# Performance work log

Measured on AMD Instinct MI355X. Metric: run time of the kernel, lower is better.

## Reference

```python
import jax, jax.numpy as jnp
import numpy as np
from jax.scipy.special import gammaln

N_VOXELS = 500_000
SPATIAL_DIM = 256
N_STUDY = 1000
MOD_DIM = 64


def setup_inputs() -> dict:
    key = jax.random.key(0)
    ks = jax.random.split(key, 8)
    coef_spline_bases = jax.random.uniform(ks[0], (N_VOXELS, SPATIAL_DIM), dtype=jnp.float32)
    moderators_g0 = jax.random.uniform(ks[1], (N_STUDY, MOD_DIM), dtype=jnp.float32)
    moderators_g1 = jax.random.uniform(ks[2], (N_STUDY, MOD_DIM), dtype=jnp.float32)
    foci_per_voxel_g0 = jax.random.randint(ks[3], (N_VOXELS, 1), 0, 4).astype(jnp.float32)
    foci_per_voxel_g1 = jax.random.randint(ks[4], (N_VOXELS, 1), 0, 4).astype(jnp.float32)
    # Linear weights init: uniform(-0.01, 0.01) as in the torch module
    spatial_coef = jax.random.uniform(ks[5], (2, SPATIAL_DIM), dtype=jnp.float32, minval=-0.01, maxval=0.01)
    moderators_coef = jax.random.uniform(ks[6], (1, MOD_DIM), dtype=jnp.float32, minval=-0.01, maxval=0.01)
    # overdispersion init 0.01 -> sqrt = 0.1 per group
    overdispersion_sqrt = jnp.full((2,), 0.1, dtype=jnp.float32)
    return {
        "coef_spline_bases": coef_spline_bases,
        "moderators_g0": moderators_g0,
        "moderators_g1": moderators_g1,
        "foci_per_voxel_g0": foci_per_voxel_g0,
        "foci_per_voxel_g1": foci_per_voxel_g1,
        "spatial_coef": spatial_coef,
        "moderators_coef": moderators_coef,
        "overdispersion_sqrt": overdispersion_sqrt,
    }


def _three_term(y, r):
    # Fused, vectorized equivalent of the per-count python loop:
    # every voxel with y >= 1 contributes lgamma(y+r) - lgamma(y+1) - lgamma(r) exactly once.
    terms = gammaln(y + r) - gammaln(y + 1.0) - gammaln(jnp.broadcast_to(r, y.shape))
    return jnp.sum(jnp.where(y > 0, terms, 0.0))


def _group_log_l(coef_spline_bases, w_spatial, moderators, wm, y, s):
    # w_spatial: [D], wm: [1, M], y: [V, 1], s: scalar overdispersion_sqrt
    v = 1.0 / (s * s)                                    # 1 / overdispersion
    mu_spatial = jnp.exp(coef_spline_bases @ w_spatial[:, None])   # [V, 1]
    mu_mod = jnp.exp(moderators @ wm.T)                  # [S, 1]
    sum_m = jnp.sum(mu_mod)
    sum_m2 = jnp.sum(mu_mod ** 2)
    numerator = mu_spatial ** 2 * sum_m2                 # [V, 1]
    denominator = mu_spatial ** 2 * sum_m ** 2           # [V, 1]
    p = numerator / (v * mu_spatial * sum_m + numerator) # [V, 1]
    r = v * denominator / numerator                      # [V, 1] (constant per group)
    return _three_term(y, r) + jnp.sum(r * jnp.log(1.0 - p) + y * jnp.log(p))


def reference(coef_spline_bases, moderators_g0, moderators_g1,
              foci_per_voxel_g0, foci_per_voxel_g1,
              spatial_coef, moderators_coef, overdispersion_sqrt):
    ll0 = _group_log_l(coef_spline_bases, spatial_coef[0], moderators_g0,
                       moderators_coef, foci_per_voxel_g0, overdispersion_sqrt[0])
    ll1 = _group_log_l(coef_spline_bases, spatial_coef[1], moderators_g1,
                       moderators_coef, foci_per_voxel_g1, overdispersion_sqrt[1])
    return -(ll0 + ll1)
```

## Files before the change

### kernel.cpp

```cpp
#include <hip/hip_runtime.h>
#include <math.h>

#define NV 500000
#define SD 256
#define NS 1000
#define MD 64

__global__ void prep_kernel(const float* __restrict__ mod0,
                            const float* __restrict__ mod1,
                            const float* __restrict__ wm,
                            const float* __restrict__ over,
                            double* __restrict__ acc,
                            float* __restrict__ sc) {
    __shared__ float s_wm[MD];
    __shared__ float4 buf[256];
    const int tid = threadIdx.x;
    if (tid < MD) s_wm[tid] = wm[tid];
    __syncthreads();

    float sm0 = 0.f, sq0 = 0.f, sm1 = 0.f, sq1 = 0.f;
    for (int j = tid; j < NS; j += 256) {
        const float* r0 = mod0 + j * MD;
        const float* r1 = mod1 + j * MD;
        float d0 = 0.f, d1 = 0.f;
        #pragma unroll 8
        for (int k = 0; k < MD; ++k) {
            d0 += r0[k] * s_wm[k];
            d1 += r1[k] * s_wm[k];
        }
        float m0 = expf(d0), m1 = expf(d1);
        sm0 += m0; sq0 += m0 * m0;
        sm1 += m1; sq1 += m1 * m1;
    }
    buf[tid] = make_float4(sm0, sq0, sm1, sq1);
    __syncthreads();
    for (int s = 128; s > 0; s >>= 1) {
        if (tid < s) {
            float4 a = buf[tid], b = buf[tid + s];
            buf[tid] = make_float4(a.x + b.x, a.y + b.y, a.z + b.z, a.w + b.w);
        }
        __syncthreads();
    }
    if (tid == 0) {
        const float4 t = buf[0];
        const float summ[2] = { t.x, t.z };
        const float sumq[2] = { t.y, t.w };
        for (int g = 0; g < 2; ++g) {
            const float s_ = over[g];
            const float v  = 1.0f / (s_ * s_);
            const float r  = v * summ[g] * summ[g] / sumq[g];
            sc[g * 8 + 0] = v;
            sc[g * 8 + 1] = summ[g];
            sc[g * 8 + 2] = sumq[g];
            sc[g * 8 + 3] = r;
            const float lgr = lgammaf(r);
            sc[g * 8 + 4] = 0.0f;
            sc[g * 8 + 5] = lgammaf(1.0f + r) - lgammaf(2.0f) - lgr;
            sc[g * 8 + 6] = lgammaf(2.0f + r) - lgammaf(3.0f) - lgr;
            sc[g * 8 + 7] = lgammaf(3.0f + r) - lgammaf(4.0f) - lgr;
        }
        acc[0] = 0.0;
    }
}

__global__ void main_kernel(const float* __restrict__ csb,
                            const float* __restrict__ f0,
                            const float* __restrict__ f1,
                            const float* __restrict__ spatial,
                            const float* __restrict__ sc,
                            double* __restrict__ acc) {
    const int lane = threadIdx.x & 63;
    const int wib  = threadIdx.x >> 6;
    const int gw   = blockIdx.x * (blockDim.x >> 6) + wib;
    const int nw   = gridDim.x * (blockDim.x >> 6);

    const float4 w0 = reinterpret_cast<const float4*>(spatial)[lane];
    const float4 w1 = reinterpret_cast<const float4*>(spatial + SD)[lane];

    const float v0 = sc[0],  smA = sc[1],  sqA = sc[2],  rA = sc[3];
    const float tA1 = sc[5], tA2 = sc[6],  tA3 = sc[7];
    const float v1 = sc[8],  smB = sc[9],  sqB = sc[10], rB = sc[11];
    const float tB1 = sc[13], tB2 = sc[14], tB3 = sc[15];

    double accl = 0.0;
    const int nchunks = (NV + 63) >> 6;
    for (int c = gw; c < nchunks; c += nw) {
        const int base = c << 6;
        const float* rowbase = csb + (size_t)base * SD;
        float dot0 = 0.0f, dot1 = 0.0f;
        #pragma unroll 4
        for (int j = 0; j < 64; ++j) {
            float d0 = 0.0f, d1 = 0.0f;
            if (base + j < NV) {
                const float4 a = *(reinterpret_cast<const float4*>(rowbase + (size_t)j * SD) + lane);
                d0 = a.x * w0.x + a.y * w0.y + a.z * w0.z + a.w * w0.w;
                d1 = a.x * w1.x + a.y * w1.y + a.z * w1.z + a.w * w1.w;
            }
            #pragma unroll
            for (int off = 32; off > 0; off >>= 1) {
                d0 += __shfl_xor(d0, off, 64);
                d1 += __shfl_xor(d1, off, 64);
            }
            if (lane == j) { dot0 = d0; dot1 = d1; }
        }
        const int vox = base + lane;
        if (vox < NV) {
            const float y0 = f0[vox];
            const float y1 = f1[vox];
            float mu  = expf(dot0);
            float num = mu * mu * sqA;
            float den = v0 * mu * smA + num;
            float p   = num / den;
            int   yi  = (int)y0;
            float tt  = (yi == 1) ? tA1 : (yi == 2) ? tA2 : (yi == 3) ? tA3 : 0.0f;
            const float c0 = rA * logf(1.0f - p) + y0 * logf(p) + tt;
            mu  = expf(dot1);
            num = mu * mu * sqB;
            den = v1 * mu * smB + num;
            p   = num / den;
            yi  = (int)y1;
            tt  = (yi == 1) ? tB1 : (yi == 2) ? tB2 : (yi == 3) ? tB3 : 0.0f;
            const float c1 = rB * logf(1.0f - p) + y1 * logf(p) + tt;
            accl += (double)c0 + (double)c1;
        }
    }

    __shared__ double sred[256];
    sred[threadIdx.x] = accl;
    __syncthreads();
    for (int s = 128; s > 0; s >>= 1) {
        if (threadIdx.x < s) sred[threadIdx.x] += sred[threadIdx.x + s];
        __syncthreads();
    }
    if (threadIdx.x == 0) {
        unsafeAtomicAdd(acc, sred[0]);
    }
}

__global__ void fin_kernel(const double* __restrict__ acc, float* __restrict__ out) {
    if (threadIdx.x == 0 && blockIdx.x == 0) out[0] = -(float)acc[0];
}

extern "C" void kernel_launch(void* const* d_in, const int* in_sizes, int n_in,
                              void* d_out, int out_size, void* d_ws, size_t ws_size,
                              hipStream_t stream) {
    const float* csb     = (const float*)d_in[0];
    const float* mod0    = (const float*)d_in[1];
    const float* mod1    = (const float*)d_in[2];
    const float* f0      = (const float*)d_in[3];
    const float* f1      = (const float*)d_in[4];
    const float* spatial = (const float*)d_in[5];
    const float* wm      = (const float*)d_in[6];
    const float* over    = (const float*)d_in[7];
    float*  out = (float*)d_out;
    double* acc = (double*)d_ws;
    float*  sc  = (float*)((char*)d_ws + 16);

    prep_kernel<<<1, 256, 0, stream>>>(mod0, mod1, wm, over, acc, sc);
    main_kernel<<<2048, 256, 0, stream>>>(csb, f0, f1, spatial, sc, acc);
    fin_kernel<<<1, 64, 0, stream>>>(acc, out);
}
```

Baseline: 704.0 us.

## Split each row across 4 lanes to cut cross-lane shuffle reductions

Changes the dot-product mapping so each group of 4 lanes handles one voxel row (16 rows per pass, 4 passes per 64-row chunk), with weights staged in LDS. This replaces 64 full 6-step wave reductions per chunk with 2-step partial reductions plus a gather shuffle, cutting shuffle/ALU overhead in a memory-bound loop. In exchange, each lane's loads now stride within a row rather than being fully coalesced across the wave, and weights are read from LDS every iteration.

Result: no change. 708.9 us (+0.7%).

```diff
diff --git a/kernel.cpp b/kernel.cpp
--- a/kernel.cpp
+++ b/kernel.cpp
@@ -69,13 +69,24 @@
                             const float* __restrict__ spatial,
                             const float* __restrict__ sc,
                             double* __restrict__ acc) {
-    const int lane = threadIdx.x & 63;
-    const int wib  = threadIdx.x >> 6;
+    __shared__ float4 s_w0[64];
+    __shared__ float4 s_w1[64];
+    __shared__ double sred[256];
+
+    const int tid = threadIdx.x;
+    if (tid < 64) {
+        s_w0[tid] = reinterpret_cast<const float4*>(spatial)[tid];
+        s_w1[tid] = reinterpret_cast<const float4*>(spatial + SD)[tid];
+    }
+    __syncthreads();
+
+    const int lane = tid & 63;
+    const int q    = lane & 3;
+    const int rr   = lane >> 2;
+    const int wib  = tid >> 6;
     const int gw   = blockIdx.x * (blockDim.x >> 6) + wib;
     const int nw   = gridDim.x * (blockDim.x >> 6);
-
-    const float4 w0 = reinterpret_cast<const float4*>(spatial)[lane];
-    const float4 w1 = reinterpret_cast<const float4*>(spatial + SD)[lane];
+    const int srcl = (lane & 15) << 2;
 
     const float v0 = sc[0],  smA = sc[1],  sqA = sc[2],  rA = sc[3];
     const float tA1 = sc[5], tA2 = sc[6],  tA3 = sc[7];
@@ -86,22 +97,33 @@
     const int nchunks = (NV + 63) >> 6;
     for (int c = gw; c < nchunks; c += nw) {
         const int base = c << 6;
-        const float* rowbase = csb + (size_t)base * SD;
-        float dot0 = 0.0f, dot1 = 0.0f;
-        #pragma unroll 4
-        for (int j = 0; j < 64; ++j) {
-            float d0 = 0.0f, d1 = 0.0f;
-            if (base + j < NV) {
-                const float4 a = *(reinterpret_cast<const float4*>(rowbase + (size_t)j * SD) + lane);
-                d0 = a.x * w0.x + a.y * w0.y + a.z * w0.z + a.w * w0.w;
-                d1 = a.x * w1.x + a.y * w1.y + a.z * w1.z + a.w * w1.w;
+        float dot0 = 0.f, dot1 = 0.f;
+        #pragma unroll
+        for (int p = 0; p < 4; ++p) {
+            const int row = base + (p << 4) + rr;
+            float d0e = 0.f, d0o = 0.f, d1e = 0.f, d1o = 0.f;
+            if (row < NV) {
+                const float* rb = csb + (size_t)row * SD + (q << 2);
+                #pragma unroll 4
+                for (int i = 0; i < 16; ++i) {
+                    const float4 a  = *reinterpret_cast<const float4*>(rb + (i << 4));
+                    const float4 wa = s_w0[(i << 2) + q];
+                    const float4 wb = s_w1[(i << 2) + q];
+                    d0e = fmaf(a.x, wa.x, d0e); d0o = fmaf(a.y, wa.y, d0o);
+                    d0e = fmaf(a.z, wa.z, d0e); d0o = fmaf(a.w, wa.w, d0o);
+                    d1e = fmaf(a.x, wb.x, d1e); d1o = fmaf(a.y, wb.y, d1o);
+                    d1e = fmaf(a.z, wb.z, d1e); d1o = fmaf(a.w, wb.w, d1o);
+                }
             }
-            #pragma unroll
-            for (int off = 32; off > 0; off >>= 1) {
-                d0 += __shfl_xor(d0, off, 64);
-                d1 += __shfl_xor(d1, off, 64);
-            }
-            if (lane == j) { dot0 = d0; dot1 = d1; }
+            float d0 = d0e + d0o;
+            float d1 = d1e + d1o;
+            d0 += __shfl_xor(d0, 1, 64);
+            d0 += __shfl_xor(d0, 2, 64);
+            d1 += __shfl_xor(d1, 1, 64);
+            d1 += __shfl_xor(d1, 2, 64);
+            const float g0 = __shfl(d0, srcl, 64);
+            const float g1 = __shfl(d1, srcl, 64);
+            if ((lane >> 4) == p) { dot0 = g0; dot1 = g1; }
         }
         const int vox = base + lane;
         if (vox < NV) {
@@ -110,29 +132,28 @@
             float mu  = expf(dot0);
             float num = mu * mu * sqA;
             float den = v0 * mu * smA + num;
-            float p   = num / den;
+            float pp  = num / den;
             int   yi  = (int)y0;
             float tt  = (yi == 1) ? tA1 : (yi == 2) ? tA2 : (yi == 3) ? tA3 : 0.0f;
-            const float c0 = rA * logf(1.0f - p) + y0 * logf(p) + tt;
+            const float c0 = rA * logf(1.0f - pp) + y0 * logf(pp) + tt;
             mu  = expf(dot1);
             num = mu * mu * sqB;
             den = v1 * mu * smB + num;
-            p   = num / den;
+            pp  = num / den;
             yi  = (int)y1;
             tt  = (yi == 1) ? tB1 : (yi == 2) ? tB2 : (yi == 3) ? tB3 : 0.0f;
-            const float c1 = rB * logf(1.0f - p) + y1 * logf(p) + tt;
+            const float c1 = rB * logf(1.0f - pp) + y1 * logf(pp) + tt;
             accl += (double)c0 + (double)c1;
         }
     }
 
-    __shared__ double sred[256];
-    sred[threadIdx.x] = accl;
+    sred[tid] = accl;
     __syncthreads();
     for (int s = 128; s > 0; s >>= 1) {
-        if (threadIdx.x < s) sred[threadIdx.x] += sred[threadIdx.x + s];
+        if (tid < s) sred[tid] += sred[tid + s];
         __syncthreads();
     }
-    if (threadIdx.x == 0) {
+    if (tid == 0) {
         unsafeAtomicAdd(acc, sred[0]);
     }
 }
```
